# Kernel tuning notes

Hardware: AMD Instinct MI355X
Metric: run time of the kernel (lower is better)

## Reference

```python
import jax, jax.numpy as jnp
import numpy as np

T, B, I, H = 2048, 64, 256, 256


def setup_inputs() -> dict:
    key = jax.random.key(0)
    ks = jax.random.split(key, 7)
    s = 1.0 / np.sqrt(H)  # torch LSTMCell init scale
    return {
        "input": jax.random.normal(ks[0], (T, B, I), dtype=jnp.float32),
        "h0": jax.random.normal(ks[1], (B, H), dtype=jnp.float32),
        "c0": jax.random.normal(ks[2], (B, H), dtype=jnp.float32),
        "W_ih": jax.random.uniform(ks[3], (4 * H, I), jnp.float32, -s, s),
        "W_hh": jax.random.uniform(ks[4], (4 * H, H), jnp.float32, -s, s),
        "b_ih": jax.random.uniform(ks[5], (4 * H,), jnp.float32, -s, s),
        "b_hh": jax.random.uniform(ks[6], (4 * H,), jnp.float32, -s, s),
    }


def reference(input, h0, c0, W_ih, W_hh, b_ih, b_hh):
    # Precompute the input contribution for all timesteps in one big GEMM:
    # [T,B,I] @ [I,4H] -> [T,B,4H]
    x_gates = jnp.einsum("tbi,gi->tbg", input, W_ih) + b_ih + b_hh

    def step(carry, xg):
        h, c = carry
        gates = xg + h @ W_hh.T  # [B,4H]
        i, f, g, o = jnp.split(gates, 4, axis=-1)  # torch gate order i,f,g,o
        i = jax.nn.sigmoid(i)
        f = jax.nn.sigmoid(f)
        g = jnp.tanh(g)
        o = jax.nn.sigmoid(o)
        c_new = f * c + i * g
        h_new = o * jnp.tanh(c_new)
        return (h_new, c_new), h_new

    (h_T, c_T), outputs = jax.lax.scan(step, (h0, c0), x_gates)
    return outputs, (h_T, c_T)
```

## Files before the change

### kernel.cpp

```cpp
#include <hip/hip_runtime.h>


#define TT 2048
#define BB 64
#define HH 256
#define GG 1024

#define EXCH_OFF 0
#define CST_OFF 0x40000
#define XG_OFF 0x50000

#define BM 128
#define BN 128
#define BK 64
#define LDT 132

__device__ __forceinline__ float sigm(float x) { return 1.0f / (1.0f + __expf(-x)); }
__device__ __forceinline__ float tanh_(float x) {
  float e = __expf(2.0f * x);
  return 1.0f - 2.0f / (e + 1.0f);
}

__device__ __forceinline__ unsigned int pkbf(float a, float b) {
  unsigned int ua = __float_as_uint(a), ub = __float_as_uint(b);
  ua = (ua + 0x7FFFu + ((ua >> 16) & 1u)) >> 16;
  ub = (ub + 0x7FFFu + ((ub >> 16) & 1u)) >> 16;
  return ua | (ub << 16);
}

__global__ __launch_bounds__(256, 2) void lstm_xgates(
    const float* __restrict__ xin,
    const float* __restrict__ Wih,
    const float* __restrict__ bih, const float* __restrict__ bhh,
    float* __restrict__ xg,
    int t0, int ct)
{
  const int rows = ct * BB;
  const int tid = (int)threadIdx.x;
  const int mb = (int)blockIdx.x >> 3;
  const int cb = (int)blockIdx.x & 7;
  const int row0 = mb * BM;
  const int col0 = cb * BN;

  __shared__ __align__(16) float As[BK][LDT];
  __shared__ __align__(16) float Bs[BK][LDT];

  const int sc = tid & 15;
  const int sr = tid >> 4;
  const int tm = tid >> 4;
  const int tn = tid & 15;

  const float* xbase = xin + (size_t)t0 * BB * HH;

  float4 xa[8], wb[8];
#pragma unroll
  for (int i = 0; i < 8; ++i) {
    int gr = row0 + sr + 16 * i;
    int grc = gr < rows ? gr : 0;
    xa[i] = *(const float4*)(xbase + (size_t)grc * HH + 4 * sc);
    wb[i] = *(const float4*)(Wih + (size_t)(col0 + sr + 16 * i) * HH + 4 * sc);
  }

  float acc[8][8];
#pragma unroll
  for (int i = 0; i < 8; ++i)
#pragma unroll
    for (int j = 0; j < 8; ++j) acc[i][j] = 0.f;

  const int KT = HH / BK;
  for (int kt = 0; kt < KT; ++kt) {
#pragma unroll
    for (int i = 0; i < 8; ++i) {
      int r = sr + 16 * i;
      As[4 * sc + 0][r] = xa[i].x;
      As[4 * sc + 1][r] = xa[i].y;
      As[4 * sc + 2][r] = xa[i].z;
      As[4 * sc + 3][r] = xa[i].w;
      Bs[4 * sc + 0][r] = wb[i].x;
      Bs[4 * sc + 1][r] = wb[i].y;
      Bs[4 * sc + 2][r] = wb[i].z;
      Bs[4 * sc + 3][r] = wb[i].w;
    }
    __syncthreads();

    if (kt + 1 < KT) {
      const int k0 = (kt + 1) * BK;
#pragma unroll
      for (int i = 0; i < 8; ++i) {
        int gr = row0 + sr + 16 * i;
        int grc = gr < rows ? gr : 0;
        xa[i] = *(const float4*)(xbase + (size_t)grc * HH + k0 + 4 * sc);
        wb[i] = *(const float4*)(Wih + (size_t)(col0 + sr + 16 * i) * HH + k0 + 4 * sc);
      }
    }

#pragma unroll 4
    for (int k = 0; k < BK; ++k) {
      float4 a0 = *(const float4*)(&As[k][8 * tm]);
      float4 a1 = *(const float4*)(&As[k][8 * tm + 4]);
      float4 b0 = *(const float4*)(&Bs[k][4 * tn]);
      float4 b1 = *(const float4*)(&Bs[k][64 + 4 * tn]);
      const float av[8] = {a0.x, a0.y, a0.z, a0.w, a1.x, a1.y, a1.z, a1.w};
      const float bv[8] = {b0.x, b0.y, b0.z, b0.w, b1.x, b1.y, b1.z, b1.w};
#pragma unroll
      for (int i = 0; i < 8; ++i)
#pragma unroll
        for (int j = 0; j < 8; ++j)
          acc[i][j] = fmaf(av[i], bv[j], acc[i][j]);
    }
    __syncthreads();
  }

  const float4 bi0 = *(const float4*)(bih + col0 + 4 * tn);
  const float4 bh0 = *(const float4*)(bhh + col0 + 4 * tn);
  const float4 bi1 = *(const float4*)(bih + col0 + 64 + 4 * tn);
  const float4 bh1 = *(const float4*)(bhh + col0 + 64 + 4 * tn);
  const float4 bia0 = make_float4(bi0.x + bh0.x, bi0.y + bh0.y, bi0.z + bh0.z, bi0.w + bh0.w);
  const float4 bia1 = make_float4(bi1.x + bh1.x, bi1.y + bh1.y, bi1.z + bh1.z, bi1.w + bh1.w);

#pragma unroll
  for (int i = 0; i < 8; ++i) {
    int r = row0 + 8 * tm + i;
    if (r < rows) {
      float4 o0 = make_float4(acc[i][0] + bia0.x, acc[i][1] + bia0.y,
                              acc[i][2] + bia0.z, acc[i][3] + bia0.w);
      float4 o1 = make_float4(acc[i][4] + bia1.x, acc[i][5] + bia1.y,
                              acc[i][6] + bia1.z, acc[i][7] + bia1.w);
      float* op = xg + (size_t)r * GG + col0;
      *(float4*)(op + 4 * tn) = o0;
      *(float4*)(op + 64 + 4 * tn) = o1;
    }
  }
}

__global__ __launch_bounds__(1024, 1) void lstm_rec(
    const float* __restrict__ h0, const float* __restrict__ c0,
    const float* __restrict__ Whh,
    const float* __restrict__ xg,
    float* __restrict__ out,
    unsigned long long* exch,
    float* __restrict__ cstate,
    int t0, int t1)
{
  const int tid = threadIdx.x;
  const int wblk = blockIdx.x;
  const int r = wblk & 7, q = (wblk >> 3) & 3, s5 = wblk >> 5;
  const int b = 8 * s5 + r;

  const int rg = tid >> 4;
  const int kc = tid & 15;
  const int g = rg >> 4;
  const int grow0 = 256 * g + 64 * q + 4 * (rg & 15);

  unsigned int wvh[32];
  {
#pragma unroll
    for (int rr = 0; rr < 4; ++rr) {
      const float4* wp = (const float4*)(Whh + (size_t)(grow0 + rr) * HH);
#pragma unroll
      for (int j = 0; j < 4; ++j) {
        float4 w = wp[kc + 16 * j];
        wvh[8 * rr + 2 * j + 0] = pkbf(w.x, w.y);
        wvh[8 * rr + 2 * j + 1] = pkbf(w.z, w.w);
      }
    }
#pragma unroll
    for (int k = 0; k < 32; k += 4)
      asm volatile("" : "+v"(wvh[k]), "+v"(wvh[k + 1]),
                        "+v"(wvh[k + 2]), "+v"(wvh[k + 3]));
  }

  float cst = 0.f;
  if (tid < 64) {
    const int jj = 64 * q + tid;
    cst = (t0 == 0) ? c0[b * HH + jj] : cstate[b * HH + jj];
  }

  __shared__ __align__(16) float hbf[256];
  __shared__ __align__(16) float gl[256];

  unsigned long long* exb = exch + b * 512;
  const int sidx = (tid + 64 * q) & 255;

  const bool xgl = (kc == 0);
  float4 xgv = make_float4(0.f, 0.f, 0.f, 0.f), xgn1 = xgv;
  if (xgl) {
    xgv = *(const float4*)(xg + (size_t)b * GG + grow0);
    if (t0 + 1 < t1)
      xgn1 = *(const float4*)(xg + ((size_t)BB + b) * GG + grow0);
  }

  for (int t = t0; t < t1; ++t) {
    if (t == 0) {
      if (tid < 256) hbf[sidx] = h0[b * HH + sidx];
    } else if (t == t0 || (tid >= 64 && tid < 256)) {
      if (tid < 256) {
        unsigned long long* slot = exb + ((t & 1) << 8) + sidx;
        unsigned long long wd;
        do {
          wd = __hip_atomic_load(slot, __ATOMIC_RELAXED, __HIP_MEMORY_SCOPE_AGENT);
        } while ((unsigned int)(wd >> 32) != (unsigned int)t);
        union { unsigned int i; float f; } cv;
        cv.i = (unsigned int)wd;
        hbf[sidx] = cv.f;
      }
    }
    __syncthreads();

    float4 xgn2 = make_float4(0.f, 0.f, 0.f, 0.f);
    if (xgl && t + 2 < t1)
      xgn2 = *(const float4*)(xg + ((size_t)(t + 2 - t0) * BB + b) * GG + grow0);

    float ac0 = 0.f, ac1 = 0.f, ac2 = 0.f, ac3 = 0.f;
    {
      const float4* hq = (const float4*)hbf;
#pragma unroll
      for (int j = 0; j < 4; ++j) {
        float4 h4 = hq[kc + 16 * j];
#pragma unroll
        for (int rr = 0; rr < 4; ++rr) {
          const unsigned int wa = wvh[8 * rr + 2 * j + 0];
          const unsigned int wb_ = wvh[8 * rr + 2 * j + 1];
          const float w0 = __uint_as_float(wa << 16);
          const float w1 = __uint_as_float(wa & 0xFFFF0000u);
          const float w2 = __uint_as_float(wb_ << 16);
          const float w3 = __uint_as_float(wb_ & 0xFFFF0000u);
          float acc = (rr == 0) ? ac0 : (rr == 1) ? ac1 : (rr == 2) ? ac2 : ac3;
          acc = fmaf(w0, h4.x, acc);
          acc = fmaf(w1, h4.y, acc);
          acc = fmaf(w2, h4.z, acc);
          acc = fmaf(w3, h4.w, acc);
          if (rr == 0) ac0 = acc; else if (rr == 1) ac1 = acc;
          else if (rr == 2) ac2 = acc; else ac3 = acc;
        }
      }
    }
#pragma unroll
    for (int m = 1; m < 16; m <<= 1) {
      ac0 += __shfl_xor(ac0, m);
      ac1 += __shfl_xor(ac1, m);
      ac2 += __shfl_xor(ac2, m);
      ac3 += __shfl_xor(ac3, m);
    }
    if (xgl) {
      float4 o = make_float4(ac0 + xgv.x, ac1 + xgv.y, ac2 + xgv.z, ac3 + xgv.w);
      *(float4*)(&gl[4 * rg]) = o;
    }
    xgv = xgn1;
    xgn1 = xgn2;
    __syncthreads();

    if (tid < 64) {
      const float gi = gl[tid];
      const float gf = gl[64 + tid];
      const float gg = gl[128 + tid];
      const float go = gl[192 + tid];
      const float ig = sigm(gi), fg = sigm(gf), gc = tanh_(gg), og = sigm(go);
      cst = fg * cst + ig * gc;
      const float hv = og * tanh_(cst);
      const int jj = 64 * q + tid;
      union { float f; unsigned int i; } hu;
      hu.f = hv;
      __hip_atomic_exchange(exb + (((t + 1) & 1) << 8) + jj,
                            (((unsigned long long)(unsigned int)(t + 1)) << 32) | hu.i,
                            __ATOMIC_RELAXED, __HIP_MEMORY_SCOPE_AGENT);
      hbf[jj] = hv;
      __builtin_nontemporal_store(hv, &out[(size_t)t * (BB * HH) + (size_t)b * HH + jj]);
      if (t == TT - 1) {
        const size_t base = (size_t)TT * (BB * HH);
        out[base + (size_t)b * HH + jj] = hv;
        out[base + BB * HH + (size_t)b * HH + jj] = cst;
      }
      if (t == t1 - 1) cstate[b * HH + jj] = cst;
    }
  }
}

extern "C" void kernel_launch(void* const* d_in, const int* in_sizes, int n_in,
                              void* d_out, int out_size, void* d_ws, size_t ws_size,
                              hipStream_t stream) {
  const float* xin = (const float*)d_in[0];
  const float* h0 = (const float*)d_in[1];
  const float* c0 = (const float*)d_in[2];
  const float* Wih = (const float*)d_in[3];
  const float* Whh = (const float*)d_in[4];
  const float* bih = (const float*)d_in[5];
  const float* bhh = (const float*)d_in[6];
  float* out = (float*)d_out;

  char* ws = (char*)d_ws;
  unsigned long long* exch = (unsigned long long*)(ws + EXCH_OFF);
  float* cstate = (float*)(ws + CST_OFF);
  float* xg = (float*)(ws + XG_OFF);

  size_t avail = (ws_size > XG_OFF) ? (ws_size - XG_OFF) : 0;
  long chunkT = (long)(avail / ((size_t)BB * GG * sizeof(float)));
  if (chunkT > TT) chunkT = TT;
  if (chunkT < 1) chunkT = 1;

  hipMemsetAsync(ws + EXCH_OFF, 0, 0x40000, stream);
  for (int t0 = 0; t0 < TT; t0 += (int)chunkT) {
    int ct = (TT - t0 < chunkT) ? (TT - t0) : (int)chunkT;
    int mblk = (ct * BB + BM - 1) / BM;
    hipLaunchKernelGGL(lstm_xgates, dim3(mblk * (GG / BN)), dim3(256), 0, stream,
                       xin, Wih, bih, bhh, xg, t0, ct);
    hipLaunchKernelGGL(lstm_rec, dim3(256), dim3(1024), 0, stream,
                       h0, c0, Whh, xg, out, exch, cstate, t0, t0 + ct);
  }
}
```

Measured before the change: 4.953 ms.

## Fuse input-gate projection into persistent recurrent kernel with register-resident W_ih

Drops the separate input-projection GEMM kernel and the xg workspace. Each recurrent block now keeps its slice of W_ih in registers as packed bf16 and computes the x·W_ih contribution for step t+1 while it waits on step t, double-buffering x rows in shared memory. This removes the large xg write/read round trip and the extra launches. In exchange it adds register pressure and more per-step compute on the serial critical path, and W_ih is now rounded to bf16.

Result: slower. 19.48 ms (+293.2%).

```diff
diff --git a/kernel.cpp b/kernel.cpp
--- a/kernel.cpp
+++ b/kernel.cpp
@@ -7,13 +7,6 @@
 #define GG 1024
 
 #define EXCH_OFF 0
-#define CST_OFF 0x40000
-#define XG_OFF 0x50000
-
-#define BM 128
-#define BN 128
-#define BK 64
-#define LDT 132
 
 __device__ __forceinline__ float sigm(float x) { return 1.0f / (1.0f + __expf(-x)); }
 __device__ __forceinline__ float tanh_(float x) {
@@ -28,118 +21,14 @@
   return ua | (ub << 16);
 }
 
-__global__ __launch_bounds__(256, 2) void lstm_xgates(
+__global__ __launch_bounds__(1024, 1) void lstm_rec(
     const float* __restrict__ xin,
+    const float* __restrict__ h0, const float* __restrict__ c0,
     const float* __restrict__ Wih,
+    const float* __restrict__ Whh,
     const float* __restrict__ bih, const float* __restrict__ bhh,
-    float* __restrict__ xg,
-    int t0, int ct)
-{
-  const int rows = ct * BB;
-  const int tid = (int)threadIdx.x;
-  const int mb = (int)blockIdx.x >> 3;
-  const int cb = (int)blockIdx.x & 7;
-  const int row0 = mb * BM;
-  const int col0 = cb * BN;
-
-  __shared__ __align__(16) float As[BK][LDT];
-  __shared__ __align__(16) float Bs[BK][LDT];
-
-  const int sc = tid & 15;
-  const int sr = tid >> 4;
-  const int tm = tid >> 4;
-  const int tn = tid & 15;
-
-  const float* xbase = xin + (size_t)t0 * BB * HH;
-
-  float4 xa[8], wb[8];
-#pragma unroll
-  for (int i = 0; i < 8; ++i) {
-    int gr = row0 + sr + 16 * i;
-    int grc = gr < rows ? gr : 0;
-    xa[i] = *(const float4*)(xbase + (size_t)grc * HH + 4 * sc);
-    wb[i] = *(const float4*)(Wih + (size_t)(col0 + sr + 16 * i) * HH + 4 * sc);
-  }
-
-  float acc[8][8];
-#pragma unroll
-  for (int i = 0; i < 8; ++i)
-#pragma unroll
-    for (int j = 0; j < 8; ++j) acc[i][j] = 0.f;
-
-  const int KT = HH / BK;
-  for (int kt = 0; kt < KT; ++kt) {
-#pragma unroll
-    for (int i = 0; i < 8; ++i) {
-      int r = sr + 16 * i;
-      As[4 * sc + 0][r] = xa[i].x;
-      As[4 * sc + 1][r] = xa[i].y;
-      As[4 * sc + 2][r] = xa[i].z;
-      As[4 * sc + 3][r] = xa[i].w;
-      Bs[4 * sc + 0][r] = wb[i].x;
-      Bs[4 * sc + 1][r] = wb[i].y;
-      Bs[4 * sc + 2][r] = wb[i].z;
-      Bs[4 * sc + 3][r] = wb[i].w;
-    }
-    __syncthreads();
-
-    if (kt + 1 < KT) {
-      const int k0 = (kt + 1) * BK;
-#pragma unroll
-      for (int i = 0; i < 8; ++i) {
-        int gr = row0 + sr + 16 * i;
-        int grc = gr < rows ? gr : 0;
-        xa[i] = *(const float4*)(xbase + (size_t)grc * HH + k0 + 4 * sc);
-        wb[i] = *(const float4*)(Wih + (size_t)(col0 + sr + 16 * i) * HH + k0 + 4 * sc);
-      }
-    }
-
-#pragma unroll 4
-    for (int k = 0; k < BK; ++k) {
-      float4 a0 = *(const float4*)(&As[k][8 * tm]);
-      float4 a1 = *(const float4*)(&As[k][8 * tm + 4]);
-      float4 b0 = *(const float4*)(&Bs[k][4 * tn]);
-      float4 b1 = *(const float4*)(&Bs[k][64 + 4 * tn]);
-      const float av[8] = {a0.x, a0.y, a0.z, a0.w, a1.x, a1.y, a1.z, a1.w};
-      const float bv[8] = {b0.x, b0.y, b0.z, b0.w, b1.x, b1.y, b1.z, b1.w};
-#pragma unroll
-      for (int i = 0; i < 8; ++i)
-#pragma unroll
-        for (int j = 0; j < 8; ++j)
-          acc[i][j] = fmaf(av[i], bv[j], acc[i][j]);
-    }
-    __syncthreads();
-  }
-
-  const float4 bi0 = *(const float4*)(bih + col0 + 4 * tn);
-  const float4 bh0 = *(const float4*)(bhh + col0 + 4 * tn);
-  const float4 bi1 = *(const float4*)(bih + col0 + 64 + 4 * tn);
-  const float4 bh1 = *(const float4*)(bhh + col0 + 64 + 4 * tn);
-  const float4 bia0 = make_float4(bi0.x + bh0.x, bi0.y + bh0.y, bi0.z + bh0.z, bi0.w + bh0.w);
-  const float4 bia1 = make_float4(bi1.x + bh1.x, bi1.y + bh1.y, bi1.z + bh1.z, bi1.w + bh1.w);
-
-#pragma unroll
-  for (int i = 0; i < 8; ++i) {
-    int r = row0 + 8 * tm + i;
-    if (r < rows) {
-      float4 o0 = make_float4(acc[i][0] + bia0.x, acc[i][1] + bia0.y,
-                              acc[i][2] + bia0.z, acc[i][3] + bia0.w);
-      float4 o1 = make_float4(acc[i][4] + bia1.x, acc[i][5] + bia1.y,
-                              acc[i][6] + bia1.z, acc[i][7] + bia1.w);
-      float* op = xg + (size_t)r * GG + col0;
-      *(float4*)(op + 4 * tn) = o0;
-      *(float4*)(op + 64 + 4 * tn) = o1;
-    }
-  }
-}
-
-__global__ __launch_bounds__(1024, 1) void lstm_rec(
-    const float* __restrict__ h0, const float* __restrict__ c0,
-    const float* __restrict__ Whh,
-    const float* __restrict__ xg,
     float* __restrict__ out,
     unsigned long long* exch,
-    float* __restrict__ cstate,
     int t0, int t1)
 {
   const int tid = threadIdx.x;
@@ -152,45 +41,106 @@
   const int g = rg >> 4;
   const int grow0 = 256 * g + 64 * q + 4 * (rg & 15);
 
-  unsigned int wvh[32];
+  unsigned int whh[32], wih[32];
   {
 #pragma unroll
     for (int rr = 0; rr < 4; ++rr) {
-      const float4* wp = (const float4*)(Whh + (size_t)(grow0 + rr) * HH);
+      const float4* hp = (const float4*)(Whh + (size_t)(grow0 + rr) * HH);
+      const float4* ip = (const float4*)(Wih + (size_t)(grow0 + rr) * HH);
 #pragma unroll
       for (int j = 0; j < 4; ++j) {
-        float4 w = wp[kc + 16 * j];
-        wvh[8 * rr + 2 * j + 0] = pkbf(w.x, w.y);
-        wvh[8 * rr + 2 * j + 1] = pkbf(w.z, w.w);
-      }
-    }
-#pragma unroll
-    for (int k = 0; k < 32; k += 4)
-      asm volatile("" : "+v"(wvh[k]), "+v"(wvh[k + 1]),
-                        "+v"(wvh[k + 2]), "+v"(wvh[k + 3]));
+        float4 wh = hp[kc + 16 * j];
+        float4 wi = ip[kc + 16 * j];
+        whh[8 * rr + 2 * j + 0] = pkbf(wh.x, wh.y);
+        whh[8 * rr + 2 * j + 1] = pkbf(wh.z, wh.w);
+        wih[8 * rr + 2 * j + 0] = pkbf(wi.x, wi.y);
+        wih[8 * rr + 2 * j + 1] = pkbf(wi.z, wi.w);
+      }
+    }
+  }
+
+  const bool xgl = (kc == 0);
+  float4 bias4 = make_float4(0.f, 0.f, 0.f, 0.f);
+  if (xgl) {
+    float4 bi = *(const float4*)(bih + grow0);
+    float4 bh = *(const float4*)(bhh + grow0);
+    bias4 = make_float4(bi.x + bh.x, bi.y + bh.y, bi.z + bh.z, bi.w + bh.w);
   }
 
   float cst = 0.f;
-  if (tid < 64) {
-    const int jj = 64 * q + tid;
-    cst = (t0 == 0) ? c0[b * HH + jj] : cstate[b * HH + jj];
-  }
+  if (tid < 64) cst = c0[b * HH + 64 * q + tid];
 
   __shared__ __align__(16) float hbf[256];
   __shared__ __align__(16) float gl[256];
+  __shared__ __align__(16) float xbf[2][256];
 
   unsigned long long* exb = exch + b * 512;
   const int sidx = (tid + 64 * q) & 255;
 
-  const bool xgl = (kc == 0);
-  float4 xgv = make_float4(0.f, 0.f, 0.f, 0.f), xgn1 = xgv;
-  if (xgl) {
-    xgv = *(const float4*)(xg + (size_t)b * GG + grow0);
+  if (tid < 64) {
+    *(float4*)&xbf[t0 & 1][4 * tid] =
+        *(const float4*)(xin + ((size_t)t0 * BB + b) * HH + 4 * tid);
     if (t0 + 1 < t1)
-      xgn1 = *(const float4*)(xg + ((size_t)BB + b) * GG + grow0);
+      *(float4*)&xbf[(t0 + 1) & 1][4 * tid] =
+          *(const float4*)(xin + ((size_t)(t0 + 1) * BB + b) * HH + 4 * tid);
+  }
+  __syncthreads();
+
+  float xc0 = 0.f, xc1 = 0.f, xc2 = 0.f, xc3 = 0.f;
+  {
+    const float4* xq = (const float4*)&xbf[t0 & 1][0];
+#pragma unroll
+    for (int j = 0; j < 4; ++j) {
+      float4 x4 = xq[kc + 16 * j];
+#pragma unroll
+      for (int rr = 0; rr < 4; ++rr) {
+        const unsigned int wa = wih[8 * rr + 2 * j + 0];
+        const unsigned int wb_ = wih[8 * rr + 2 * j + 1];
+        const float w0 = __uint_as_float(wa << 16);
+        const float w1 = __uint_as_float(wa & 0xFFFF0000u);
+        const float w2 = __uint_as_float(wb_ << 16);
+        const float w3 = __uint_as_float(wb_ & 0xFFFF0000u);
+        float acc = (rr == 0) ? xc0 : (rr == 1) ? xc1 : (rr == 2) ? xc2 : xc3;
+        acc = fmaf(w0, x4.x, acc);
+        acc = fmaf(w1, x4.y, acc);
+        acc = fmaf(w2, x4.z, acc);
+        acc = fmaf(w3, x4.w, acc);
+        if (rr == 0) xc0 = acc; else if (rr == 1) xc1 = acc;
+        else if (rr == 2) xc2 = acc; else xc3 = acc;
+      }
+    }
   }
 
   for (int t = t0; t < t1; ++t) {
+    float4 xpre = make_float4(0.f, 0.f, 0.f, 0.f);
+    if (tid < 64 && t + 2 < t1)
+      xpre = *(const float4*)(xin + ((size_t)(t + 2) * BB + b) * HH + 4 * tid);
+
+    float xn0 = 0.f, xn1 = 0.f, xn2 = 0.f, xn3 = 0.f;
+    if (t + 1 < t1) {
+      const float4* xq = (const float4*)&xbf[(t + 1) & 1][0];
+#pragma unroll
+      for (int j = 0; j < 4; ++j) {
+        float4 x4 = xq[kc + 16 * j];
+#pragma unroll
+        for (int rr = 0; rr < 4; ++rr) {
+          const unsigned int wa = wih[8 * rr + 2 * j + 0];
+          const unsigned int wb_ = wih[8 * rr + 2 * j + 1];
+          const float w0 = __uint_as_float(wa << 16);
+          const float w1 = __uint_as_float(wa & 0xFFFF0000u);
+          const float w2 = __uint_as_float(wb_ << 16);
+          const float w3 = __uint_as_float(wb_ & 0xFFFF0000u);
+          float acc = (rr == 0) ? xn0 : (rr == 1) ? xn1 : (rr == 2) ? xn2 : xn3;
+          acc = fmaf(w0, x4.x, acc);
+          acc = fmaf(w1, x4.y, acc);
+          acc = fmaf(w2, x4.z, acc);
+          acc = fmaf(w3, x4.w, acc);
+          if (rr == 0) xn0 = acc; else if (rr == 1) xn1 = acc;
+          else if (rr == 2) xn2 = acc; else xn3 = acc;
+        }
+      }
+    }
+
     if (t == 0) {
       if (tid < 256) hbf[sidx] = h0[b * HH + sidx];
     } else if (t == t0 || (tid >= 64 && tid < 256)) {
@@ -207,11 +157,7 @@
     }
     __syncthreads();
 
-    float4 xgn2 = make_float4(0.f, 0.f, 0.f, 0.f);
-    if (xgl && t + 2 < t1)
-      xgn2 = *(const float4*)(xg + ((size_t)(t + 2 - t0) * BB + b) * GG + grow0);
-
-    float ac0 = 0.f, ac1 = 0.f, ac2 = 0.f, ac3 = 0.f;
+    float ac0 = xc0, ac1 = xc1, ac2 = xc2, ac3 = xc3;
     {
       const float4* hq = (const float4*)hbf;
 #pragma unroll
@@ -219,8 +165,8 @@
         float4 h4 = hq[kc + 16 * j];
 #pragma unroll
         for (int rr = 0; rr < 4; ++rr) {
-          const unsigned int wa = wvh[8 * rr + 2 * j + 0];
-          const unsigned int wb_ = wvh[8 * rr + 2 * j + 1];
+          const unsigned int wa = whh[8 * rr + 2 * j + 0];
+          const unsigned int wb_ = whh[8 * rr + 2 * j + 1];
           const float w0 = __uint_as_float(wa << 16);
           const float w1 = __uint_as_float(wa & 0xFFFF0000u);
           const float w2 = __uint_as_float(wb_ << 16);
@@ -243,11 +189,12 @@
       ac3 += __shfl_xor(ac3, m);
     }
     if (xgl) {
-      float4 o = make_float4(ac0 + xgv.x, ac1 + xgv.y, ac2 + xgv.z, ac3 + xgv.w);
+      float4 o = make_float4(ac0 + bias4.x, ac1 + bias4.y,
+                             ac2 + bias4.z, ac3 + bias4.w);
       *(float4*)(&gl[4 * rg]) = o;
     }
-    xgv = xgn1;
-    xgn1 = xgn2;
+    if (tid < 64 && t + 2 < t1) *(float4*)&xbf[t & 1][4 * tid] = xpre;
+    xc0 = xn0; xc1 = xn1; xc2 = xn2; xc3 = xn3;
     __syncthreads();
 
     if (tid < 64) {
@@ -271,7 +218,6 @@
         out[base + (size_t)b * HH + jj] = hv;
         out[base + BB * HH + (size_t)b * HH + jj] = cst;
       }
-      if (t == t1 - 1) cstate[b * HH + jj] = cst;
     }
   }
 }
@@ -290,21 +236,8 @@
 
   char* ws = (char*)d_ws;
   unsigned long long* exch = (unsigned long long*)(ws + EXCH_OFF);
-  float* cstate = (float*)(ws + CST_OFF);
-  float* xg = (float*)(ws + XG_OFF);
-
-  size_t avail = (ws_size > XG_OFF) ? (ws_size - XG_OFF) : 0;
-  long chunkT = (long)(avail / ((size_t)BB * GG * sizeof(float)));
-  if (chunkT > TT) chunkT = TT;
-  if (chunkT < 1) chunkT = 1;
 
   hipMemsetAsync(ws + EXCH_OFF, 0, 0x40000, stream);
-  for (int t0 = 0; t0 < TT; t0 += (int)chunkT) {
-    int ct = (TT - t0 < chunkT) ? (TT - t0) : (int)chunkT;
-    int mblk = (ct * BB + BM - 1) / BM;
-    hipLaunchKernelGGL(lstm_xgates, dim3(mblk * (GG / BN)), dim3(256), 0, stream,
-                       xin, Wih, bih, bhh, xg, t0, ct);
-    hipLaunchKernelGGL(lstm_rec, dim3(256), dim3(1024), 0, stream,
-                       h0, c0, Whh, xg, out, exch, cstate, t0, t0 + ct);
-  }
-}
+  hipLaunchKernelGGL(lstm_rec, dim3(256), dim3(1024), 0, stream,
+                     xin, h0, c0, Wih, Whh, bih, bhh, out, exch, 0, TT);
+}
```
